# Kernel optimization log

Hardware: AMD Instinct MI355X
Metric: run time of the kernel (lower is better)

The kernel has to match this reference:

```python
import jax, jax.numpy as jnp
import numpy as np

B, LA, LQ, LO, H, OUT = 32, 2048, 64, 32, 1024, 5


def _kaiming(key, out_f, in_f):
    return jax.random.normal(key, (out_f, in_f), jnp.float32) * np.sqrt(2.0 / in_f)


def setup_inputs() -> dict:
    key = jax.random.key(0)
    ks = jax.random.split(key, 16)
    inp = {
        "article_contexts": jax.random.normal(ks[0], (B, LA, H), jnp.float32),
        "question_contexts": jax.random.normal(ks[1], (B, LQ, H), jnp.float32),
        "options_embeds": jax.random.normal(ks[2], (B, 5, LO, H), jnp.float32),
        "answer_indices": jax.random.randint(ks[3], (B,), 0, LQ),
    }
    # mlp_att (article-question attention) params
    inp["a_Qw"], inp["a_Qb"] = _kaiming(ks[4], H, H), jnp.zeros((H,), jnp.float32)
    inp["a_Kw"], inp["a_Kb"] = _kaiming(ks[5], H, H), jnp.zeros((H,), jnp.float32)
    inp["a_Vw"], inp["a_Vb"] = _kaiming(ks[6], H, H), jnp.zeros((H,), jnp.float32)
    inp["a_vw"], inp["a_vb"] = _kaiming(ks[7], 1, H), jnp.zeros((1,), jnp.float32)
    # dot_layer (option attention) params
    inp["d_Qw"], inp["d_Qb"] = _kaiming(ks[8], H, H), jnp.zeros((H,), jnp.float32)
    inp["d_Kw"], inp["d_Kb"] = _kaiming(ks[9], H, H), jnp.zeros((H,), jnp.float32)
    inp["d_Vw"], inp["d_Vb"] = _kaiming(ks[10], H, H), jnp.zeros((H,), jnp.float32)
    inp["d_vw"], inp["d_vb"] = _kaiming(ks[11], 1, H), jnp.zeros((1,), jnp.float32)
    # final linear: hidden_size*5 -> output_dim
    inp["f_w"], inp["f_b"] = _kaiming(ks[12], OUT, 5 * H), jnp.zeros((OUT,), jnp.float32)
    return inp


def _mlp_att(Q, K, V, Qw, Qb, Kw, Kb, Vw, Vb, vw, vb):
    # Q: [B, H]; K, V: [B, (..opt..), L, H]. Dropout is identity (eval mode).
    Qp = Q @ Qw.T + Qb                      # [B, H]
    Kp = K @ Kw.T + Kb                      # [..., L, H]
    Vp = V @ Vw.T + Vb                      # [..., L, H]
    while Qp.ndim < Kp.ndim:
        Qp = Qp[..., None, :]
    M = jnp.tanh(Qp + Kp)                   # [..., L, H]
    scores = jax.nn.softmax(M @ vw.T + vb, axis=-2)  # softmax over L, [..., L, 1]
    return jnp.sum(Vp * scores, axis=-2)    # [..., H]


def reference(article_contexts, question_contexts, options_embeds, answer_indices,
              a_Qw, a_Qb, a_Kw, a_Kb, a_Vw, a_Vb, a_vw, a_vb,
              d_Qw, d_Qb, d_Kw, d_Kb, d_Vw, d_Vb, d_vw, d_vb,
              f_w, f_b):
    b = article_contexts.shape[0]
    # gather question context at the answer index -> [B, H]
    oqc = question_contexts[jnp.arange(b), answer_indices]
    # article-question additive attention -> [B, H]
    aq = _mlp_att(oqc, article_contexts, article_contexts,
                  a_Qw, a_Qb, a_Kw, a_Kb, a_Vw, a_Vb, a_vw, a_vb)
    # per-option additive attention, vectorized over the 5 options -> [B, 5, H]
    feats = _mlp_att(aq, options_embeds, options_embeds,
                     d_Qw, d_Qb, d_Kw, d_Kb, d_Vw, d_Vb, d_vw, d_vb)
    # concat options along feature dim, final linear -> [B, OUT]
    logits = feats.reshape(b, -1) @ f_w.T + f_b
    return logits
```

## Files before the change

kernel.cpp:

```cpp
#include <hip/hip_runtime.h>
#include <hip/hip_bf16.h>
#include <math.h>

#define HDIM 1024
#define NB 32
#define LA 2048
#define LO 32

typedef __attribute__((ext_vector_type(8))) short bf16x8;
typedef __attribute__((ext_vector_type(4))) float f32x4;
typedef unsigned int u32;

__device__ __forceinline__ float tanh_fast(float x){
    return 2.0f / (1.0f + __expf(-2.0f * x)) - 1.0f;
}

__device__ __forceinline__ void load_lds16(const void* gptr, void* lptr){
    __builtin_amdgcn_global_load_lds(
        (const __attribute__((address_space(1))) u32*)gptr,
        (__attribute__((address_space(3))) u32*)lptr, 16, 0, 0);
}

__global__ void zero_kernel(float* __restrict__ p, int n){
    int i = blockIdx.x * blockDim.x + threadIdx.x;
    int stride = gridDim.x * blockDim.x;
    for (; i < n; i += stride) p[i] = 0.0f;
}

__global__ void conv_bf16_kernel(const float* __restrict__ in, __hip_bfloat16* __restrict__ out, long n){
    long i = ((long)blockIdx.x * blockDim.x + threadIdx.x) * 4;
    long stride = (long)gridDim.x * blockDim.x * 4;
    for (; i < n; i += stride){
        float4 v = *(const float4*)(in + i);
        union { __hip_bfloat16 h[4]; short4 s; } u;
        u.h[0] = __float2bfloat16(v.x); u.h[1] = __float2bfloat16(v.y);
        u.h[2] = __float2bfloat16(v.z); u.h[3] = __float2bfloat16(v.w);
        *(short4*)(out + i) = u.s;
    }
}

__global__ void conv2_bf16_kernel(const float* __restrict__ in0, __hip_bfloat16* __restrict__ out0, long n0,
                                  const float* __restrict__ in1, __hip_bfloat16* __restrict__ out1, long n1){
    if (blockIdx.x < 64){
        long i = ((long)blockIdx.x * blockDim.x + threadIdx.x) * 4;
        long stride = 64L * blockDim.x * 4;
        for (; i < n0; i += stride){
            float4 v = *(const float4*)(in0 + i);
            union { __hip_bfloat16 h[4]; short4 s; } u;
            u.h[0] = __float2bfloat16(v.x); u.h[1] = __float2bfloat16(v.y);
            u.h[2] = __float2bfloat16(v.z); u.h[3] = __float2bfloat16(v.w);
            *(short4*)(out0 + i) = u.s;
        }
    } else {
        long i = ((long)(blockIdx.x - 64) * blockDim.x + threadIdx.x) * 4;
        long stride = 320L * blockDim.x * 4;
        for (; i < n1; i += stride){
            float4 v = *(const float4*)(in1 + i);
            union { __hip_bfloat16 h[4]; short4 s; } u;
            u.h[0] = __float2bfloat16(v.x); u.h[1] = __float2bfloat16(v.y);
            u.h[2] = __float2bfloat16(v.z); u.h[3] = __float2bfloat16(v.w);
            *(short4*)(out1 + i) = u.s;
        }
    }
}

__global__ __launch_bounds__(256) void proj_q_kernel(
    const float* __restrict__ question, const int* __restrict__ ans,
    const float* __restrict__ W, const float* __restrict__ bias, float* __restrict__ out){
    __shared__ float xin[HDIM];
    const int g = blockIdx.x, tid = threadIdx.x;
    const int lane = tid & 63, wave = tid >> 6;
    const float* in = question + ((size_t)g * 64 + ans[g]) * HDIM;
    *(float4*)&xin[tid * 4] = *(const float4*)&in[tid * 4];
    __syncthreads();
    float4 xv[4];
    #pragma unroll
    for (int c = 0; c < 4; c++) xv[c] = *(const float4*)&xin[(c * 64 + lane) * 4];
    const int hbase = blockIdx.y * 64 + wave * 16;
    #pragma unroll 4
    for (int r = 0; r < 16; r++){
        int h = hbase + r;
        const float* Wr = W + (size_t)h * HDIM;
        float p = 0.f;
        #pragma unroll
        for (int c = 0; c < 4; c++){
            float4 wv = *(const float4*)&Wr[(c * 64 + lane) * 4];
            p = fmaf(xv[c].x, wv.x, p); p = fmaf(xv[c].y, wv.y, p);
            p = fmaf(xv[c].z, wv.z, p); p = fmaf(xv[c].w, wv.w, p);
        }
        #pragma unroll
        for (int off = 1; off < 64; off <<= 1) p += __shfl_xor(p, off, 64);
        if (lane == 0) out[(size_t)g * HDIM + h] = p + bias[h];
    }
}

__global__ __launch_bounds__(256) void proj_kernel(
    const float* __restrict__ in, const float* __restrict__ W,
    const float* __restrict__ bias, float* __restrict__ out){
    __shared__ float xin[HDIM];
    const int g = blockIdx.x, tid = threadIdx.x;
    const int lane = tid & 63, wave = tid >> 6;
    *(float4*)&xin[tid * 4] = *(const float4*)&in[(size_t)g * HDIM + tid * 4];
    __syncthreads();
    float4 xv[4];
    #pragma unroll
    for (int c = 0; c < 4; c++) xv[c] = *(const float4*)&xin[(c * 64 + lane) * 4];
    const int hbase = blockIdx.y * 64 + wave * 16;
    #pragma unroll 4
    for (int r = 0; r < 16; r++){
        int h = hbase + r;
        const float* Wr = W + (size_t)h * HDIM;
        float p = 0.f;
        #pragma unroll
        for (int c = 0; c < 4; c++){
            float4 wv = *(const float4*)&Wr[(c * 64 + lane) * 4];
            p = fmaf(xv[c].x, wv.x, p); p = fmaf(xv[c].y, wv.y, p);
            p = fmaf(xv[c].z, wv.z, p); p = fmaf(xv[c].w, wv.w, p);
        }
        #pragma unroll
        for (int off = 1; off < 64; off <<= 1) p += __shfl_xor(p, off, 64);
        if (lane == 0) out[(size_t)g * HDIM + h] = p + bias[h];
    }
}

__global__ __launch_bounds__(512, 2) void score_mfma8p(
    const __hip_bfloat16* __restrict__ X, const __hip_bfloat16* __restrict__ Kw,
    const float* __restrict__ Kb, const float* __restrict__ Qp,
    const float* __restrict__ vw, float* __restrict__ s,
    int rows_per_batch)
{
    __shared__ __align__(16) char lds[131072];
    const int tid = threadIdx.x;
    const int lane = tid & 63, wid = tid >> 6;
    const int wm = wid >> 2, wn = wid & 3;
    const int lr = lane & 15, lg = lane >> 4;

    const int na = gridDim.x >> 2;
    const int bid = blockIdx.x;
    const int xcd = bid & 7, seq = bid >> 3;
    const int a_idx = xcd * (na >> 3) + (seq >> 2);
    const int h_idx = seq & 3;
    const int a0 = a_idx * 256, h0 = h_idx * 256;

    f32x4 acc[8][4] = {};
    bf16x8 av[8], bv[4];

    const int rA = tid >> 2;
    const int csw = ((tid & 3) * 16) ^ (((rA >> 1) & 3) << 4);
    const char* pA = (const char*)Kw + (size_t)(h0 + rA) * 2048 + csw;
    const char* pB = (const char*)X  + (size_t)(a0 + rA) * 2048 + csw;
    char* dst0 = lds + tid * 16;

    int aoff[8], boff[4];
    #pragma unroll
    for (int hf = 0; hf < 8; hf++){
        int rw = wm * 128 + hf * 16 + lr;
        aoff[hf] = rw * 64 + ((lg * 16) ^ (((rw >> 1) & 3) << 4));
    }
    #pragma unroll
    for (int af = 0; af < 4; af++){
        int rw = wn * 64 + af * 16 + lr;
        boff[af] = 16384 + rw * 64 + ((lg * 16) ^ (((rw >> 1) & 3) << 4));
    }

#define ISSUE_PAIR(j) do { \
    const int _base = (((j) >> 1) & 1) * 65536 + ((j) & 1) * 32768; \
    const size_t _ko = (size_t)(((j) >> 1) * 128 + ((j) & 1) * 64); \
    load_lds16(pA + _ko, dst0 + _base); \
    load_lds16(pA + _ko + 262144, dst0 + _base + 8192); \
    load_lds16(pB + _ko, dst0 + _base + 16384); \
    load_lds16(pB + _ko + 262144, dst0 + _base + 24576); } while(0)

#define READS_PAIR(k) do { \
    const int _base = (((k) >> 1) & 1) * 65536 + ((k) & 1) * 32768; \
    _Pragma("unroll") \
    for (int hf = 0; hf < 8; hf++) av[hf] = *(const bf16x8*)(lds + _base + aoff[hf]); \
    _Pragma("unroll") \
    for (int af = 0; af < 4; af++) bv[af] = *(const bf16x8*)(lds + _base + boff[af]); } while(0)

#define MFMA32() do { \
    asm volatile("s_waitcnt lgkmcnt(0)" ::: "memory"); \
    __builtin_amdgcn_sched_barrier(0); \
    __builtin_amdgcn_s_setprio(1); \
    _Pragma("unroll") \
    for (int hf = 0; hf < 8; hf++) \
        _Pragma("unroll") \
        for (int af = 0; af < 4; af++) \
            acc[hf][af] = __builtin_amdgcn_mfma_f32_16x16x32_bf16(av[hf], bv[af], acc[hf][af], 0, 0, 0); \
    __builtin_amdgcn_s_setprio(0); } while(0)

    ISSUE_PAIR(0); ISSUE_PAIR(1); ISSUE_PAIR(2);

    #pragma unroll 2
    for (int k = 0; k < 29; ++k){
        asm volatile("s_waitcnt vmcnt(8)" ::: "memory");
        __builtin_amdgcn_s_barrier();
        ISSUE_PAIR(k + 3);
        READS_PAIR(k);
        MFMA32();
    }
    {
        asm volatile("s_waitcnt vmcnt(8)" ::: "memory");
        __builtin_amdgcn_s_barrier();
        READS_PAIR(29);
        MFMA32();
    }
    {
        asm volatile("s_waitcnt vmcnt(4)" ::: "memory");
        __builtin_amdgcn_s_barrier();
        READS_PAIR(30);
        MFMA32();
    }
    {
        asm volatile("s_waitcnt vmcnt(0)" ::: "memory");
        __builtin_amdgcn_s_barrier();
        READS_PAIR(31);
        MFMA32();
    }

    const int b = a0 / rows_per_batch;
    float part[4] = {0.f, 0.f, 0.f, 0.f};
    #pragma unroll
    for (int hf = 0; hf < 8; hf++){
        int hbase = h0 + wm * 128 + hf * 16 + lg * 4;
        float4 kb4 = *(const float4*)(Kb + hbase);
        float4 qp4 = *(const float4*)(Qp + (size_t)b * HDIM + hbase);
        float4 vw4 = *(const float4*)(vw + hbase);
        float q0v = kb4.x + qp4.x, q1v = kb4.y + qp4.y;
        float q2v = kb4.z + qp4.z, q3v = kb4.w + qp4.w;
        #pragma unroll
        for (int af = 0; af < 4; af++){
            part[af] += tanh_fast(acc[hf][af][0] + q0v) * vw4.x;
            part[af] += tanh_fast(acc[hf][af][1] + q1v) * vw4.y;
            part[af] += tanh_fast(acc[hf][af][2] + q2v) * vw4.z;
            part[af] += tanh_fast(acc[hf][af][3] + q3v) * vw4.w;
        }
    }
    #pragma unroll
    for (int af = 0; af < 4; af++){
        float p = part[af];
        p += __shfl_xor(p, 16, 64);
        p += __shfl_xor(p, 32, 64);
        if (lane < 16)
            atomicAdd(&s[a0 + wn * 64 + af * 16 + lr], p);
    }
#undef ISSUE_PAIR
#undef READS_PAIR
#undef MFMA32
}

#define SBM 128
#define SBN 128
__global__ __launch_bounds__(256) void score_mfma_kernel(
    const __hip_bfloat16* __restrict__ X, const __hip_bfloat16* __restrict__ Kw,
    const float* __restrict__ Kb, const float* __restrict__ Qp,
    const float* __restrict__ vw, float* __restrict__ s,
    int row_off, int rows_per_batch)
{
    __shared__ __align__(16) __hip_bfloat16 As[SBM][32];
    __shared__ __align__(16) __hip_bfloat16 Bs[SBN][32];
    const int tid = threadIdx.x;
    const int lane = tid & 63, wid = tid >> 6;
    const int wm = wid >> 1, wn = wid & 1;
    const int row0 = blockIdx.x * SBM;
    const int h0 = blockIdx.y * SBN;
    const int lr = lane & 15, lg = lane >> 4;

    f32x4 acc[4][4] = {};

    for (int k0 = 0; k0 < HDIM; k0 += 32){
        #pragma unroll
        for (int l = 0; l < 2; l++){
            int f = tid + l * 256;
            int r = f >> 2, c8 = (f & 3) * 8;
            load_lds16(X + (size_t)(row0 + r) * HDIM + k0 + c8, &As[0][0] + f * 8);
            load_lds16(Kw + (size_t)(h0 + r) * HDIM + k0 + c8, &Bs[0][0] + f * 8);
        }
        __syncthreads();
        bf16x8 a[4], b[4];
        #pragma unroll
        for (int i = 0; i < 4; i++)
            a[i] = *(const bf16x8*)&As[wm * 64 + i * 16 + lr][lg * 8];
        #pragma unroll
        for (int j = 0; j < 4; j++)
            b[j] = *(const bf16x8*)&Bs[wn * 64 + j * 16 + lr][lg * 8];
        #pragma unroll
        for (int i = 0; i < 4; i++)
            #pragma unroll
            for (int j = 0; j < 4; j++)
                acc[i][j] = __builtin_amdgcn_mfma_f32_16x16x32_bf16(a[i], b[j], acc[i][j], 0, 0, 0);
        __syncthreads();
    }

    float kbv[4], vwv[4];
    #pragma unroll
    for (int j = 0; j < 4; j++){
        int h = h0 + wn * 64 + j * 16 + lr;
        kbv[j] = Kb[h]; vwv[j] = vw[h];
    }
    #pragma unroll
    for (int i = 0; i < 4; i++){
        #pragma unroll
        for (int reg = 0; reg < 4; reg++){
            int r = row0 + wm * 64 + i * 16 + lg * 4 + reg;
            int gr = row_off + r;
            int bb = gr / rows_per_batch;
            const float* Qpb = Qp + (size_t)bb * HDIM;
            float p = 0.f;
            #pragma unroll
            for (int j = 0; j < 4; j++){
                int h = h0 + wn * 64 + j * 16 + lr;
                p += tanh_fast(acc[i][j][reg] + kbv[j] + Qpb[h]) * vwv[j];
            }
            #pragma unroll
            for (int off = 1; off < 16; off <<= 1) p += __shfl_xor(p, off, 16);
            if (lr == 0) atomicAdd(&s[gr], p);
        }
    }
}

__global__ void softmax_kernel(float* __restrict__ s, int Rg){
    __shared__ float red[4];
    int g = blockIdx.x, tid = threadIdx.x;
    float* sg = s + (size_t)g * Rg;
    float m = -INFINITY;
    for (int i = tid; i < Rg; i += 256) m = fmaxf(m, sg[i]);
    #pragma unroll
    for (int off = 32; off > 0; off >>= 1) m = fmaxf(m, __shfl_down(m, off, 64));
    if ((tid & 63) == 0) red[tid >> 6] = m;
    __syncthreads();
    m = fmaxf(fmaxf(red[0], red[1]), fmaxf(red[2], red[3]));
    __syncthreads();
    float sum = 0.f;
    for (int i = tid; i < Rg; i += 256){ float e = __expf(sg[i] - m); sg[i] = e; sum += e; }
    #pragma unroll
    for (int off = 32; off > 0; off >>= 1) sum += __shfl_down(sum, off, 64);
    if ((tid & 63) == 0) red[tid >> 6] = sum;
    __syncthreads();
    float inv = 1.0f / (red[0] + red[1] + red[2] + red[3]);
    for (int i = tid; i < Rg; i += 256) sg[i] *= inv;
}

__global__ __launch_bounds__(256) void wsum_art_v(
    const __hip_bfloat16* __restrict__ X, const float* __restrict__ sc,
    float* __restrict__ out){
    __shared__ float scs[256];
    const int g = blockIdx.x, ic = blockIdx.y, tid = threadIdx.x;
    scs[tid] = sc[(size_t)g * LA + ic * 256 + tid];
    __syncthreads();
    const __hip_bfloat16* Xg = X + ((size_t)g * LA + ic * 256) * HDIM + tid * 4;
    float a0 = 0.f, a1 = 0.f, a2 = 0.f, a3 = 0.f;
    for (int i = 0; i < 256; i++){
        short4 v = *(const short4*)(Xg + (size_t)i * HDIM);
        float w = scs[i];
        a0 = fmaf(w, __bfloat162float(*(const __hip_bfloat16*)&v.x), a0);
        a1 = fmaf(w, __bfloat162float(*(const __hip_bfloat16*)&v.y), a1);
        a2 = fmaf(w, __bfloat162float(*(const __hip_bfloat16*)&v.z), a2);
        a3 = fmaf(w, __bfloat162float(*(const __hip_bfloat16*)&v.w), a3);
    }
    float* o = out + (size_t)g * HDIM + tid * 4;
    atomicAdd(o + 0, a0); atomicAdd(o + 1, a1);
    atomicAdd(o + 2, a2); atomicAdd(o + 3, a3);
}

__global__ __launch_bounds__(256) void wsum_opt_v(
    const __hip_bfloat16* __restrict__ X, const float* __restrict__ sc,
    float* __restrict__ out){
    __shared__ float scs[LO];
    const int g = blockIdx.x, tid = threadIdx.x;
    if (tid < LO) scs[tid] = sc[(size_t)g * LO + tid];
    __syncthreads();
    const __hip_bfloat16* Xg = X + (size_t)g * LO * HDIM + tid * 4;
    float a0 = 0.f, a1 = 0.f, a2 = 0.f, a3 = 0.f;
    for (int i = 0; i < LO; i++){
        short4 v = *(const short4*)(Xg + (size_t)i * HDIM);
        float w = scs[i];
        a0 = fmaf(w, __bfloat162float(*(const __hip_bfloat16*)&v.x), a0);
        a1 = fmaf(w, __bfloat162float(*(const __hip_bfloat16*)&v.y), a1);
        a2 = fmaf(w, __bfloat162float(*(const __hip_bfloat16*)&v.z), a2);
        a3 = fmaf(w, __bfloat162float(*(const __hip_bfloat16*)&v.w), a3);
    }
    float* o = out + (size_t)g * HDIM + tid * 4;
    o[0] = a0; o[1] = a1; o[2] = a2; o[3] = a3;
}

__global__ void final_kernel(const float* __restrict__ feats, const float* __restrict__ fw,
                             const float* __restrict__ fb, float* __restrict__ out){
    __shared__ float red[4];
    int b = blockIdx.x, tid = threadIdx.x;
    const float* fe = feats + (size_t)b * 5120;
    for (int j = 0; j < 5; j++){
        float acc = 0.f;
        for (int i = tid; i < 5120; i += 256) acc += fe[i] * fw[(size_t)j * 5120 + i];
        #pragma unroll
        for (int off = 32; off > 0; off >>= 1) acc += __shfl_down(acc, off, 64);
        if ((tid & 63) == 0) red[tid >> 6] = acc;
        __syncthreads();
        if (tid == 0) out[b * 5 + j] = fb[j] + red[0] + red[1] + red[2] + red[3];
        __syncthreads();
    }
}

extern "C" void kernel_launch(void* const* d_in, const int* in_sizes, int n_in,
                              void* d_out, int out_size, void* d_ws, size_t ws_size,
                              hipStream_t stream) {
    const float* article  = (const float*)d_in[0];
    const float* question = (const float*)d_in[1];
    const float* options  = (const float*)d_in[2];
    const int*   ans      = (const int*)d_in[3];
    const float* a_Qw = (const float*)d_in[4];  const float* a_Qb = (const float*)d_in[5];
    const float* a_Kw = (const float*)d_in[6];  const float* a_Kb = (const float*)d_in[7];
    const float* a_Vw = (const float*)d_in[8];  const float* a_Vb = (const float*)d_in[9];
    const float* a_vw = (const float*)d_in[10];
    const float* d_Qw = (const float*)d_in[12]; const float* d_Qb = (const float*)d_in[13];
    const float* d_Kw = (const float*)d_in[14]; const float* d_Kb = (const float*)d_in[15];
    const float* d_Vw = (const float*)d_in[16]; const float* d_Vb = (const float*)d_in[17];
    const float* d_vw = (const float*)d_in[18];
    const float* f_w  = (const float*)d_in[20]; const float* f_b  = (const float*)d_in[21];
    float* out = (float*)d_out;

    float* ws = (float*)d_ws;
    float* qp_a  = ws + 32768;
    float* aq    = ws + 65536;
    float* qp_d  = ws + 98304;
    float* feats = ws + 131072;
    float* s_art = ws + 294912;
    float* s_opt = ws + 360448;
    float* w_art = ws + 365568;
    float* wd    = ws + 398336;
    __hip_bfloat16* kwa_bf = (__hip_bfloat16*)(ws + 562176);
    __hip_bfloat16* kwd_bf = kwa_bf + 1048576;
    __hip_bfloat16* opt_bf = kwd_bf + 1048576;
    __hip_bfloat16* art_bf = opt_bf + 5242880;

    zero_kernel<<<128, 256, 0, stream>>>(s_art, 103424);
    proj_q_kernel<<<dim3(NB, 16), 256, 0, stream>>>(question, ans, a_Qw, a_Qb, qp_a);
    conv_bf16_kernel<<<64, 256, 0, stream>>>(a_Kw, kwa_bf, 1048576);
    conv_bf16_kernel<<<1024, 256, 0, stream>>>(article, art_bf, (long)NB * LA * HDIM);

    score_mfma8p<<<(NB * LA / 256) * 4, 512, 0, stream>>>(
        art_bf, kwa_bf, a_Kb, qp_a, a_vw, s_art, LA);
    softmax_kernel<<<NB, 256, 0, stream>>>(s_art, LA);
    wsum_art_v<<<dim3(NB, 8), 256, 0, stream>>>(art_bf, s_art, w_art);
    proj_kernel<<<dim3(NB, 16), 256, 0, stream>>>(w_art, a_Vw, a_Vb, aq);

    proj_kernel<<<dim3(NB, 16), 256, 0, stream>>>(aq, d_Qw, d_Qb, qp_d);
    conv2_bf16_kernel<<<384, 256, 0, stream>>>(d_Kw, kwd_bf, 1048576,
                                               options, opt_bf, 5242880);
    score_mfma_kernel<<<dim3((NB * 5 * LO) / SBM, HDIM / SBN), 256, 0, stream>>>(
        opt_bf, kwd_bf, d_Kb, qp_d, d_vw, s_opt, 0, 5 * LO);
    softmax_kernel<<<NB * 5, 256, 0, stream>>>(s_opt, LO);
    wsum_opt_v<<<NB * 5, 256, 0, stream>>>(opt_bf, s_opt, wd);
    proj_kernel<<<dim3(NB * 5, 16), 256, 0, stream>>>(wd, d_Vw, d_Vb, feats);
    final_kernel<<<NB, 256, 0, stream>>>(feats, f_w, f_b, out);
}
```

Before: 427.6 us.

## Merge init kernels, fuse back-to-back projections, fold option softmax into weighted sum

Combines zeroing, the question projection and all bf16 conversions into one block-partitioned init kernel, cutting several launches. Chains the a_Vw and d_Qw projections in a single per-batch kernel that keeps the intermediate vector in shared memory. Folds the option-score softmax into the weighted-sum kernel. The fused projection uses only 32 blocks, each streaming both full weight matrices, so it gives up a lot of parallelism compared with the previous 512-block grids.

Measured after the change: 754.5 us. 1.76x slower.

```diff
diff --git a/kernel.cpp b/kernel.cpp
--- a/kernel.cpp
+++ b/kernel.cpp
@@ -21,15 +21,11 @@
         (__attribute__((address_space(3))) u32*)lptr, 16, 0, 0);
 }
 
-__global__ void zero_kernel(float* __restrict__ p, int n){
-    int i = blockIdx.x * blockDim.x + threadIdx.x;
-    int stride = gridDim.x * blockDim.x;
-    for (; i < n; i += stride) p[i] = 0.0f;
-}
-
-__global__ void conv_bf16_kernel(const float* __restrict__ in, __hip_bfloat16* __restrict__ out, long n){
-    long i = ((long)blockIdx.x * blockDim.x + threadIdx.x) * 4;
-    long stride = (long)gridDim.x * blockDim.x * 4;
+__device__ __forceinline__ void conv_range(const float* __restrict__ in,
+                                           __hip_bfloat16* __restrict__ out,
+                                           long n, int nblk, int lb){
+    long i = ((long)lb * 256 + threadIdx.x) * 4;
+    long stride = (long)nblk * 256 * 4;
     for (; i < n; i += stride){
         float4 v = *(const float4*)(in + i);
         union { __hip_bfloat16 h[4]; short4 s; } u;
@@ -39,48 +35,80 @@
     }
 }
 
-__global__ void conv2_bf16_kernel(const float* __restrict__ in0, __hip_bfloat16* __restrict__ out0, long n0,
-                                  const float* __restrict__ in1, __hip_bfloat16* __restrict__ out1, long n1){
-    if (blockIdx.x < 64){
-        long i = ((long)blockIdx.x * blockDim.x + threadIdx.x) * 4;
-        long stride = 64L * blockDim.x * 4;
-        for (; i < n0; i += stride){
-            float4 v = *(const float4*)(in0 + i);
-            union { __hip_bfloat16 h[4]; short4 s; } u;
-            u.h[0] = __float2bfloat16(v.x); u.h[1] = __float2bfloat16(v.y);
-            u.h[2] = __float2bfloat16(v.z); u.h[3] = __float2bfloat16(v.w);
-            *(short4*)(out0 + i) = u.s;
-        }
-    } else {
-        long i = ((long)(blockIdx.x - 64) * blockDim.x + threadIdx.x) * 4;
-        long stride = 320L * blockDim.x * 4;
-        for (; i < n1; i += stride){
-            float4 v = *(const float4*)(in1 + i);
-            union { __hip_bfloat16 h[4]; short4 s; } u;
-            u.h[0] = __float2bfloat16(v.x); u.h[1] = __float2bfloat16(v.y);
-            u.h[2] = __float2bfloat16(v.z); u.h[3] = __float2bfloat16(v.w);
-            *(short4*)(out1 + i) = u.s;
-        }
-    }
-}
-
-__global__ __launch_bounds__(256) void proj_q_kernel(
+__global__ __launch_bounds__(256) void mega_init_kernel(
+    const float* __restrict__ article, __hip_bfloat16* __restrict__ art_bf,
+    float* __restrict__ zbase,
     const float* __restrict__ question, const int* __restrict__ ans,
-    const float* __restrict__ W, const float* __restrict__ bias, float* __restrict__ out){
+    const float* __restrict__ a_Qw, const float* __restrict__ a_Qb,
+    float* __restrict__ qp_a,
+    const float* __restrict__ a_Kw, __hip_bfloat16* __restrict__ kwa_bf,
+    const float* __restrict__ d_Kw, __hip_bfloat16* __restrict__ kwd_bf,
+    const float* __restrict__ options, __hip_bfloat16* __restrict__ opt_bf)
+{
     __shared__ float xin[HDIM];
+    int bid = blockIdx.x;
+    const int tid = threadIdx.x;
+    if (bid < 1024){ conv_range(article, art_bf, 67108864L, 1024, bid); return; }
+    bid -= 1024;
+    if (bid < 32){
+        int i = bid * 256 + tid;
+        for (; i < 103424; i += 8192) zbase[i] = 0.f;
+        return;
+    }
+    bid -= 32;
+    if (bid < 512){
+        const int g = bid >> 4, yq = bid & 15;
+        const int lane = tid & 63, wave = tid >> 6;
+        const float* in = question + ((size_t)g * 64 + ans[g]) * HDIM;
+        *(float4*)&xin[tid * 4] = *(const float4*)&in[tid * 4];
+        __syncthreads();
+        float4 xv[4];
+        #pragma unroll
+        for (int c = 0; c < 4; c++) xv[c] = *(const float4*)&xin[(c * 64 + lane) * 4];
+        const int hbase = yq * 64 + wave * 16;
+        #pragma unroll 4
+        for (int r = 0; r < 16; r++){
+            int h = hbase + r;
+            const float* Wr = a_Qw + (size_t)h * HDIM;
+            float p = 0.f;
+            #pragma unroll
+            for (int c = 0; c < 4; c++){
+                float4 wv = *(const float4*)&Wr[(c * 64 + lane) * 4];
+                p = fmaf(xv[c].x, wv.x, p); p = fmaf(xv[c].y, wv.y, p);
+                p = fmaf(xv[c].z, wv.z, p); p = fmaf(xv[c].w, wv.w, p);
+            }
+            #pragma unroll
+            for (int off = 1; off < 64; off <<= 1) p += __shfl_xor(p, off, 64);
+            if (lane == 0) qp_a[(size_t)g * HDIM + h] = p + a_Qb[h];
+        }
+        return;
+    }
+    bid -= 512;
+    if (bid < 64){ conv_range(a_Kw, kwa_bf, 1048576L, 64, bid); return; }
+    bid -= 64;
+    if (bid < 64){ conv_range(d_Kw, kwd_bf, 1048576L, 64, bid); return; }
+    bid -= 64;
+    conv_range(options, opt_bf, 5242880L, 320, bid);
+}
+
+__global__ __launch_bounds__(256) void proj2_kernel(
+    const float* __restrict__ w_art,
+    const float* __restrict__ a_Vw, const float* __restrict__ a_Vb,
+    const float* __restrict__ d_Qw, const float* __restrict__ d_Qb,
+    float* __restrict__ qp_d)
+{
+    __shared__ float xin[HDIM];
+    __shared__ float mid[HDIM];
     const int g = blockIdx.x, tid = threadIdx.x;
     const int lane = tid & 63, wave = tid >> 6;
-    const float* in = question + ((size_t)g * 64 + ans[g]) * HDIM;
-    *(float4*)&xin[tid * 4] = *(const float4*)&in[tid * 4];
+    *(float4*)&xin[tid * 4] = *(const float4*)&w_art[(size_t)g * HDIM + tid * 4];
     __syncthreads();
     float4 xv[4];
     #pragma unroll
     for (int c = 0; c < 4; c++) xv[c] = *(const float4*)&xin[(c * 64 + lane) * 4];
-    const int hbase = blockIdx.y * 64 + wave * 16;
-    #pragma unroll 4
-    for (int r = 0; r < 16; r++){
-        int h = hbase + r;
-        const float* Wr = W + (size_t)h * HDIM;
+    for (int r = 0; r < 256; r++){
+        int h = wave * 256 + r;
+        const float* Wr = a_Vw + (size_t)h * HDIM;
         float p = 0.f;
         #pragma unroll
         for (int c = 0; c < 4; c++){
@@ -90,7 +118,25 @@
         }
         #pragma unroll
         for (int off = 1; off < 64; off <<= 1) p += __shfl_xor(p, off, 64);
-        if (lane == 0) out[(size_t)g * HDIM + h] = p + bias[h];
+        if (lane == 0) mid[h] = p + a_Vb[h];
+    }
+    __syncthreads();
+    float4 yv[4];
+    #pragma unroll
+    for (int c = 0; c < 4; c++) yv[c] = *(const float4*)&mid[(c * 64 + lane) * 4];
+    for (int r = 0; r < 256; r++){
+        int h = wave * 256 + r;
+        const float* Wr = d_Qw + (size_t)h * HDIM;
+        float p = 0.f;
+        #pragma unroll
+        for (int c = 0; c < 4; c++){
+            float4 wv = *(const float4*)&Wr[(c * 64 + lane) * 4];
+            p = fmaf(yv[c].x, wv.x, p); p = fmaf(yv[c].y, wv.y, p);
+            p = fmaf(yv[c].z, wv.z, p); p = fmaf(yv[c].w, wv.w, p);
+        }
+        #pragma unroll
+        for (int off = 1; off < 64; off <<= 1) p += __shfl_xor(p, off, 64);
+        if (lane == 0) qp_d[(size_t)g * HDIM + h] = p + d_Qb[h];
     }
 }
 
@@ -363,12 +409,20 @@
     atomicAdd(o + 2, a2); atomicAdd(o + 3, a3);
 }
 
-__global__ __launch_bounds__(256) void wsum_opt_v(
-    const __hip_bfloat16* __restrict__ X, const float* __restrict__ sc,
+__global__ __launch_bounds__(256) void wsum_opt_sm(
+    const __hip_bfloat16* __restrict__ X, const float* __restrict__ sraw,
     float* __restrict__ out){
-    __shared__ float scs[LO];
+    __shared__ float raw[LO], scs[LO];
     const int g = blockIdx.x, tid = threadIdx.x;
-    if (tid < LO) scs[tid] = sc[(size_t)g * LO + tid];
+    if (tid < LO) raw[tid] = sraw[(size_t)g * LO + tid];
+    __syncthreads();
+    float m = -INFINITY;
+    #pragma unroll
+    for (int i = 0; i < LO; i++) m = fmaxf(m, raw[i]);
+    float ssum = 0.f;
+    #pragma unroll
+    for (int i = 0; i < LO; i++) ssum += __expf(raw[i] - m);
+    if (tid < LO) scs[tid] = __expf(raw[tid] - m) / ssum;
     __syncthreads();
     const __hip_bfloat16* Xg = X + (size_t)g * LO * HDIM + tid * 4;
     float a0 = 0.f, a1 = 0.f, a2 = 0.f, a3 = 0.f;
@@ -421,7 +475,6 @@
 
     float* ws = (float*)d_ws;
     float* qp_a  = ws + 32768;
-    float* aq    = ws + 65536;
     float* qp_d  = ws + 98304;
     float* feats = ws + 131072;
     float* s_art = ws + 294912;
@@ -433,24 +486,18 @@
     __hip_bfloat16* opt_bf = kwd_bf + 1048576;
     __hip_bfloat16* art_bf = opt_bf + 5242880;
 
-    zero_kernel<<<128, 256, 0, stream>>>(s_art, 103424);
-    proj_q_kernel<<<dim3(NB, 16), 256, 0, stream>>>(question, ans, a_Qw, a_Qb, qp_a);
-    conv_bf16_kernel<<<64, 256, 0, stream>>>(a_Kw, kwa_bf, 1048576);
-    conv_bf16_kernel<<<1024, 256, 0, stream>>>(article, art_bf, (long)NB * LA * HDIM);
-
+    mega_init_kernel<<<2016, 256, 0, stream>>>(
+        article, art_bf, s_art,
+        question, ans, a_Qw, a_Qb, qp_a,
+        a_Kw, kwa_bf, d_Kw, kwd_bf, options, opt_bf);
     score_mfma8p<<<(NB * LA / 256) * 4, 512, 0, stream>>>(
         art_bf, kwa_bf, a_Kb, qp_a, a_vw, s_art, LA);
     softmax_kernel<<<NB, 256, 0, stream>>>(s_art, LA);
     wsum_art_v<<<dim3(NB, 8), 256, 0, stream>>>(art_bf, s_art, w_art);
-    proj_kernel<<<dim3(NB, 16), 256, 0, stream>>>(w_art, a_Vw, a_Vb, aq);
-
-    proj_kernel<<<dim3(NB, 16), 256, 0, stream>>>(aq, d_Qw, d_Qb, qp_d);
-    conv2_bf16_kernel<<<384, 256, 0, stream>>>(d_Kw, kwd_bf, 1048576,
-                                               options, opt_bf, 5242880);
+    proj2_kernel<<<NB, 256, 0, stream>>>(w_art, a_Vw, a_Vb, d_Qw, d_Qb, qp_d);
     score_mfma_kernel<<<dim3((NB * 5 * LO) / SBM, HDIM / SBN), 256, 0, stream>>>(
         opt_bf, kwd_bf, d_Kb, qp_d, d_vw, s_opt, 0, 5 * LO);
-    softmax_kernel<<<NB * 5, 256, 0, stream>>>(s_opt, LO);
-    wsum_opt_v<<<NB * 5, 256, 0, stream>>>(opt_bf, s_opt, wd);
+    wsum_opt_sm<<<NB * 5, 256, 0, stream>>>(opt_bf, s_opt, wd);
     proj_kernel<<<dim3(NB * 5, 16), 256, 0, stream>>>(wd, d_Vw, d_Vb, feats);
     final_kernel<<<NB, 256, 0, stream>>>(feats, f_w, f_b, out);
 }
```
